# Kernel optimization log

Measured on AMD Instinct MI355X. Metric: run time of the kernel, lower is better.

## Reference

```python
import jax, jax.numpy as jnp
import numpy as np

N_NODES = 50000


def rgcn_conv(x, src, dst, edge_type, W, root, bias):
    """PyG RGCNConv: out[i] = x[i] @ root + bias + sum_r mean_{j in N_r(i)} x[j] @ W[r].
    W: [R, F_in, F_out]. Mean aggregation is per-relation (PyG default aggr='mean')."""
    num_rel = W.shape[0]
    n = x.shape[0]
    out = x @ root + bias
    x_src = x[src]  # [E, F_in] gather once
    for r in range(num_rel):  # small fixed relation count
        mask = (edge_type == r)
        msg = jnp.where(mask[:, None], x_src, 0.0) @ W[r]          # [E, F_out]
        s = jax.ops.segment_sum(msg, dst, num_segments=n)           # [N, F_out]
        c = jax.ops.segment_sum(mask.astype(x.dtype), dst, num_segments=n)  # [N]
        out = out + s / jnp.maximum(c, 1.0)[:, None]
    return out


def setup_inputs() -> dict:
    key = jax.random.key(0)
    ks = jax.random.split(key, 10)
    N, E, F_in, F_hid, F_out, R = N_NODES, 800000, 128, 128, 64, 8
    x = jax.random.normal(ks[0], (N, F_in), dtype=jnp.float32)
    edge_index = jax.random.randint(ks[1], (2, E), 0, N, dtype=jnp.int64)
    edge_type = jax.random.randint(ks[2], (E,), 0, R, dtype=jnp.int64)
    s1 = 1.0 / np.sqrt(F_in)
    s2 = 1.0 / np.sqrt(F_hid)
    W1 = jax.random.normal(ks[3], (R, F_in, F_hid), dtype=jnp.float32) * s1
    root1 = jax.random.normal(ks[4], (F_in, F_hid), dtype=jnp.float32) * s1
    b1 = jnp.zeros((F_hid,), dtype=jnp.float32)
    W2 = jax.random.normal(ks[5], (R, F_hid, F_out), dtype=jnp.float32) * s2
    root2 = jax.random.normal(ks[6], (F_hid, F_out), dtype=jnp.float32) * s2
    b2 = jnp.zeros((F_out,), dtype=jnp.float32)
    return {"x": x, "edge_index": edge_index, "edge_type": edge_type,
            "W1": W1, "root1": root1, "b1": b1,
            "W2": W2, "root2": root2, "b2": b2}


def reference(x, edge_index, edge_type, W1, root1, b1, W2, root2, b2):
    src, dst = edge_index[0], edge_index[1]
    h = jax.nn.relu(rgcn_conv(x, src, dst, edge_type, W1, root1, b1))
    out = rgcn_conv(h, src, dst, edge_type, W2, root2, b2)
    return out
```

## Files before the change

kernel.cpp:

```cpp
#include <hip/hip_runtime.h>

#define N_NODES 50000
#define N_EDGES 800000
#define R_REL   8
#define NR      (N_NODES * R_REL)

#define NBKT    196
#define BNSH    8
#define BKEYS   2048
#define BCAP    5120
#define SLAB    2048
#define BINBLK  ((N_EDGES + SLAB - 1) / SLAB)

typedef float  f32x4  __attribute__((ext_vector_type(4)));
typedef __bf16 bf16x8 __attribute__((ext_vector_type(8)));

__device__ __forceinline__ unsigned short f2bf(float f) {
    unsigned int u = __float_as_uint(f);
    u = (u + 0x7FFFu + ((u >> 16) & 1u)) >> 16;
    return (unsigned short)u;
}
__device__ __forceinline__ float bflo(unsigned int u) { return __uint_as_float(u << 16); }
__device__ __forceinline__ float bfhi(unsigned int u) { return __uint_as_float(u & 0xFFFF0000u); }

__device__ __forceinline__ void acc16(float* a, uint4 u0, uint4 u1) {
    a[0]  += bflo(u0.x);   a[1]  += bfhi(u0.x);
    a[2]  += bflo(u0.y);   a[3]  += bfhi(u0.y);
    a[4]  += bflo(u0.z);   a[5]  += bfhi(u0.z);
    a[6]  += bflo(u0.w);   a[7]  += bfhi(u0.w);
    a[8]  += bflo(u1.x);   a[9]  += bfhi(u1.x);
    a[10] += bflo(u1.y);   a[11] += bfhi(u1.y);
    a[12] += bflo(u1.z);   a[13] += bfhi(u1.z);
    a[14] += bflo(u1.w);   a[15] += bfhi(u1.w);
}


__global__ __launch_bounds__(256) void k_binA(
    const int* __restrict__ src, const int* __restrict__ dst,
    const int* __restrict__ et, int* __restrict__ gcur,
    uint2* __restrict__ gbin)
{
    __shared__ int hist[NBKT];
    __shared__ int base[NBKT];
    const int t = threadIdx.x;
    const int e0 = blockIdx.x * SLAB;
    for (int i = t; i < NBKT; i += 256) hist[i] = 0;
    __syncthreads();
#pragma unroll
    for (int i = 0; i < SLAB / 256; ++i) {
        int e = e0 + i * 256 + t;
        if (e < N_EDGES) atomicAdd(&hist[dst[e] >> BNSH], 1);
    }
    __syncthreads();
    for (int i = t; i < NBKT; i += 256) {
        int h = hist[i];
        base[i] = (h > 0) ? atomicAdd(&gcur[i], h) : 0;
        hist[i] = 0;
    }
    __syncthreads();
#pragma unroll
    for (int i = 0; i < SLAB / 256; ++i) {
        int e = e0 + i * 256 + t;
        if (e < N_EDGES) {
            int d = dst[e];
            int b = d >> BNSH;
            int sub = atomicAdd(&hist[b], 1);
            gbin[b * BCAP + base[b] + sub] =
                make_uint2((unsigned)src[e], (unsigned)(d * 8 + et[e]));
        }
    }
}

__global__ __launch_bounds__(256) void k_bcount_scan(
    const int* __restrict__ gcur, const uint2* __restrict__ gbin,
    int* __restrict__ offs, int* __restrict__ bsum)
{
    __shared__ int lc[BKEYS];
    __shared__ int sd[256];
    const int t = threadIdx.x;
    const int b = blockIdx.x;
    for (int i = t; i < BKEYS; i += 256) lc[i] = 0;
    __syncthreads();
    const int n = gcur[b];
    const uint2* rec = gbin + (size_t)b * BCAP;
    const int kbase = b * BKEYS;
    for (int j = t; j < n; j += 256)
        atomicAdd(&lc[rec[j].y - kbase], 1);
    __syncthreads();
    const int base = t * 8;
    int v[8];
    int tot = 0;
#pragma unroll
    for (int i = 0; i < 8; i++) {
        int xv = lc[base + i];
        v[i] = tot;
        tot += xv;
    }
    sd[t] = tot;
    __syncthreads();
    for (int off = 1; off < 256; off <<= 1) {
        int y = (t >= off) ? sd[t - off] : 0;
        __syncthreads();
        sd[t] += y;
        __syncthreads();
    }
    int excl = sd[t] - tot;
#pragma unroll
    for (int i = 0; i < 8; i++) {
        int k = kbase + base + i;
        if (k < NR) offs[k] = v[i] + excl;
    }
    if (t == 255) bsum[b] = sd[255];
}

__global__ __launch_bounds__(256) void k_bscat_final(
    const int* __restrict__ gcur, const uint2* __restrict__ gbin,
    const int* __restrict__ bsum, int* __restrict__ offs,
    int* __restrict__ srcS)
{
    __shared__ int obase[BKEYS];
    __shared__ int cur[BKEYS];
    __shared__ int sd[256];
    __shared__ int sadd;
    const int t = threadIdx.x;
    const int b = blockIdx.x;

    int v = (t < NBKT) ? bsum[t] : 0;
    sd[t] = v;
    __syncthreads();
    for (int off = 1; off < 256; off <<= 1) {
        int y = (t >= off) ? sd[t - off] : 0;
        __syncthreads();
        sd[t] += y;
        __syncthreads();
    }
    if (t == b) sadd = sd[t] - v;
    __syncthreads();
    const int add = sadd;

    const int kbase = b * BKEYS;
    for (int i = t; i < BKEYS; i += 256) {
        int k = kbase + i;
        int o = ((k < NR) ? offs[k] : 0) + add;
        obase[i] = o;
        cur[i] = 0;
        if (k < NR) offs[k] = o;
    }
    if (b == 0 && t == 0) offs[NR] = N_EDGES;
    __syncthreads();

    const int n = gcur[b];
    const uint2* rec = gbin + (size_t)b * BCAP;
    for (int j = t; j < n; j += 256) {
        uint2 r = rec[j];
        int li = r.y - kbase;
        int sub = atomicAdd(&cur[li], 1);
        srcS[obase[li] + sub] = (int)r.x;
    }
}


#define W1_ELEMS (9 * 128 * 128)
#define W2_ELEMS (9 * 64 * 128)
#define N4       (N_NODES * 32)

__global__ __launch_bounds__(256) void k_cvtw(
    const float* __restrict__ x, unsigned short* __restrict__ xb,
    const float* __restrict__ root1, const float* __restrict__ W1,
    const float* __restrict__ root2, const float* __restrict__ W2,
    unsigned short* __restrict__ Wt1, unsigned short* __restrict__ Wt2,
    int* __restrict__ gcur)
{
    const int idx = blockIdx.x * 256 + threadIdx.x;
    if (blockIdx.x == 0) gcur[threadIdx.x] = 0;
    if (idx < N4) {
        float4 v = *(const float4*)(x + (size_t)idx * 4);
        ushort4 o;
        o.x = f2bf(v.x); o.y = f2bf(v.y); o.z = f2bf(v.z); o.w = f2bf(v.w);
        *(ushort4*)(xb + (size_t)idx * 4) = o;
    }
    if (idx < W1_ELEMS) {
        int j    = idx & 7;
        int lane = (idx >> 3) & 63;
        int r    = idx >> 9;
        int nb   = r & 7;
        int r2   = r >> 3;
        int kk   = r2 & 3;
        int seg  = r2 >> 2;
        int k = kk * 32 + (lane >> 4) * 8 + j;
        int n = nb * 16 + (lane & 15);
        float v = (seg == 0) ? root1[k * 128 + n] : W1[((seg - 1) * 128 + k) * 128 + n];
        Wt1[idx] = f2bf(v);
    } else if (idx < W1_ELEMS + W2_ELEMS) {
        int i2   = idx - W1_ELEMS;
        int j    = i2 & 7;
        int lane = (i2 >> 3) & 63;
        int r    = i2 >> 9;
        int nb   = r & 3;
        int r2   = r >> 2;
        int kk   = r2 & 3;
        int seg  = r2 >> 2;
        int k = kk * 32 + (lane >> 4) * 8 + j;
        int n = nb * 16 + (lane & 15);
        float v = (seg == 0) ? root2[k * 64 + n] : W2[((seg - 1) * 128 + k) * 64 + n];
        Wt2[i2] = f2bf(v);
    }
}


template <int FOUT, bool RELU, bool OUT_BF16>
__global__ __launch_bounds__(512) void k_fused(
    const unsigned short* __restrict__ xin,
    const unsigned short* __restrict__ WtP,
    const float* __restrict__ bias,
    const int* __restrict__ offs,
    const int* __restrict__ srcS,
    unsigned short* __restrict__ outb,
    float* __restrict__ outf)
{
    constexpr int NBt = FOUT / 16;
    __shared__ __align__(16) unsigned short As[9][16][136];

    const int t = threadIdx.x;
    const int node0 = blockIdx.x * 16;

    if (t < 128) {
        const int sr = t >> 3;
        const int sp = t & 7;
        const uint4* src = (const uint4*)(xin + (size_t)(node0 + sr) * 128 + sp * 16);
        uint4 r0 = src[0], r1 = src[1];
        uint4* d = (uint4*)&As[0][sr][sp * 16];
        d[0] = r0; d[1] = r1;
    }

    {
        const int nl  = t >> 5;
        const int rel = (t >> 2) & 7;
        const int q   = t & 3;

        const int pair = (node0 + nl) * 8 + rel;
        const int beg = offs[pair];
        const int end = offs[pair + 1];
        const int deg = end - beg;

        const unsigned short* bx = xin + q * 32;
        float a[32];
#pragma unroll
        for (int i = 0; i < 32; ++i) a[i] = 0.f;

        int j = beg;
        for (; j + 1 < end; j += 2) {
            int s0 = srcS[j];
            int s1 = srcS[j + 1];
            const uint4* p0 = (const uint4*)(bx + (size_t)s0 * 128);
            const uint4* p1 = (const uint4*)(bx + (size_t)s1 * 128);
            uint4 v0 = p0[0], v1 = p0[1], v2 = p0[2], v3 = p0[3];
            uint4 w0 = p1[0], w1 = p1[1], w2 = p1[2], w3 = p1[3];
            acc16(a, v0, v1);
            acc16(a + 16, v2, v3);
            acc16(a, w0, w1);
            acc16(a + 16, w2, w3);
        }
        if (j < end) {
            int s = srcS[j];
            const uint4* p = (const uint4*)(bx + (size_t)s * 128);
            uint4 v0 = p[0], v1 = p[1], v2 = p[2], v3 = p[3];
            acc16(a, v0, v1);
            acc16(a + 16, v2, v3);
        }

        float scl = 1.f / (float)(deg > 1 ? deg : 1);
        unsigned int pk[16];
#pragma unroll
        for (int i = 0; i < 16; ++i)
            pk[i] = (unsigned int)f2bf(a[i * 2] * scl) |
                    ((unsigned int)f2bf(a[i * 2 + 1] * scl) << 16);
        uint4* G = (uint4*)&As[1 + rel][nl][0];
        const int g0 = q * 4;
        G[(g0 + 0) ^ rel] = make_uint4(pk[0],  pk[1],  pk[2],  pk[3]);
        G[(g0 + 1) ^ rel] = make_uint4(pk[4],  pk[5],  pk[6],  pk[7]);
        G[(g0 + 2) ^ rel] = make_uint4(pk[8],  pk[9],  pk[10], pk[11]);
        G[(g0 + 3) ^ rel] = make_uint4(pk[12], pk[13], pk[14], pk[15]);
    }

    __syncthreads();

    const int lane = t & 63;
    const int w = t >> 6;
    if (w >= NBt) return;
    const int quad = lane >> 4;
    const int tc = lane & 15;

    f32x4 acc = (f32x4){0.f, 0.f, 0.f, 0.f};
    const bf16x8* Bp = (const bf16x8*)WtP;

#pragma unroll
    for (int seg = 0; seg < 9; ++seg) {
        const uint4* Ag = (const uint4*)&As[seg][tc][0];
        const int s = (seg == 0) ? 0 : (seg - 1);
#pragma unroll
        for (int kk = 0; kk < 4; ++kk) {
            bf16x8 af = *(const bf16x8*)(Ag + (((kk << 2) + quad) ^ s));
            bf16x8 bf = Bp[((seg * 4 + kk) * NBt + w) * 64 + lane];
            acc = __builtin_amdgcn_mfma_f32_16x16x32_bf16(af, bf, acc, 0, 0, 0);
        }
    }

    const int col = w * 16 + tc;
    const float bs = bias[col];
#pragma unroll
    for (int i = 0; i < 4; ++i) {
        int r = node0 + quad * 4 + i;
        float v = acc[i] + bs;
        if (RELU) v = fmaxf(v, 0.f);
        if (OUT_BF16) outb[(size_t)r * FOUT + col] = f2bf(v);
        else          outf[(size_t)r * FOUT + col] = v;
    }
}


extern "C" void kernel_launch(void* const* d_in, const int* in_sizes, int n_in,
                              void* d_out, int out_size, void* d_ws, size_t ws_size,
                              hipStream_t stream) {
    const float* x     = (const float*)d_in[0];
    const int*   ei    = (const int*)d_in[1];
    const int*   et    = (const int*)d_in[2];
    const float* W1    = (const float*)d_in[3];
    const float* root1 = (const float*)d_in[4];
    const float* b1    = (const float*)d_in[5];
    const float* W2    = (const float*)d_in[6];
    const float* root2 = (const float*)d_in[7];
    const float* b2    = (const float*)d_in[8];
    float* out = (float*)d_out;

    int* ws     = (int*)d_ws;
    int* cnt    = ws;
    int* offs   = cnt + NR;
    int* wt2buf = offs + NR + 128;
    int* bsum   = wt2buf + NR;
    int* bsum2  = bsum + 256;
    int* gcur   = bsum2 + 256;
    int* srcS   = gcur + 256;
    unsigned short* xb  = (unsigned short*)(srcS + N_EDGES);
    unsigned short* hb  = xb + (size_t)N_NODES * 128;
    uint2* gbin = (uint2*)(hb + (size_t)N_NODES * 128);
    unsigned short* Wt1 = (unsigned short*)cnt;
    unsigned short* Wt2 = (unsigned short*)wt2buf;

    k_cvtw<<<(N4 + 255) / 256, 256, 0, stream>>>(x, xb, root1, W1, root2, W2,
                                                 Wt1, Wt2, gcur);
    k_binA<<<BINBLK, 256, 0, stream>>>(ei, ei + N_EDGES, et, gcur, gbin);
    k_bcount_scan<<<NBKT, 256, 0, stream>>>(gcur, gbin, offs, bsum);
    k_bscat_final<<<NBKT, 256, 0, stream>>>(gcur, gbin, bsum, offs, srcS);

    const int NT = N_NODES / 16;

    k_fused<128, true,  true ><<<NT, 512, 0, stream>>>(xb, Wt1, b1, offs, srcS, hb, nullptr);
    k_fused<64,  false, false><<<NT, 512, 0, stream>>>(hb, Wt2, b2, offs, srcS, nullptr, out);
}
```

Baseline: 250.7 us.

## Replace global CSR build with per-tile edge bins sorted in LDS

Edges are now binned directly into fixed-capacity buckets of 16 destination nodes in a single kernel, packing source and (node, relation) into one 32-bit word. This removes the separate count/scan and scatter kernels. Each fused aggregation block then counts, scans and sorts its own bucket's edges by (node, relation) in shared memory and reads sources from LDS instead of a global CSR array. The per-bucket capacity of 512 means edges beyond it would be silently dropped on skewed graphs, and the small local sort is now done in both layers.

```diff
diff --git a/kernel.cpp b/kernel.cpp
--- a/kernel.cpp
+++ b/kernel.cpp
@@ -3,12 +3,9 @@
 #define N_NODES 50000
 #define N_EDGES 800000
 #define R_REL   8
-#define NR      (N_NODES * R_REL)
-
-#define NBKT    196
-#define BNSH    8
-#define BKEYS   2048
-#define BCAP    5120
+
+#define TNBKT   3125
+#define TCAP    512
 #define SLAB    2048
 #define BINBLK  ((N_EDGES + SLAB - 1) / SLAB)
 
@@ -35,24 +32,24 @@
 }
 
 
-__global__ __launch_bounds__(256) void k_binA(
+__global__ __launch_bounds__(256) void k_bin(
     const int* __restrict__ src, const int* __restrict__ dst,
     const int* __restrict__ et, int* __restrict__ gcur,
-    uint2* __restrict__ gbin)
+    unsigned* __restrict__ gbin)
 {
-    __shared__ int hist[NBKT];
-    __shared__ int base[NBKT];
+    __shared__ int hist[TNBKT];
+    __shared__ int base[TNBKT];
     const int t = threadIdx.x;
     const int e0 = blockIdx.x * SLAB;
-    for (int i = t; i < NBKT; i += 256) hist[i] = 0;
+    for (int i = t; i < TNBKT; i += 256) hist[i] = 0;
     __syncthreads();
 #pragma unroll
     for (int i = 0; i < SLAB / 256; ++i) {
         int e = e0 + i * 256 + t;
-        if (e < N_EDGES) atomicAdd(&hist[dst[e] >> BNSH], 1);
-    }
-    __syncthreads();
-    for (int i = t; i < NBKT; i += 256) {
+        if (e < N_EDGES) atomicAdd(&hist[dst[e] >> 4], 1);
+    }
+    __syncthreads();
+    for (int i = t; i < TNBKT; i += 256) {
         int h = hist[i];
         base[i] = (h > 0) ? atomicAdd(&gcur[i], h) : 0;
         hist[i] = 0;
@@ -63,99 +60,12 @@
         int e = e0 + i * 256 + t;
         if (e < N_EDGES) {
             int d = dst[e];
-            int b = d >> BNSH;
+            int b = d >> 4;
             int sub = atomicAdd(&hist[b], 1);
-            gbin[b * BCAP + base[b] + sub] =
-                make_uint2((unsigned)src[e], (unsigned)(d * 8 + et[e]));
-        }
-    }
-}
-
-__global__ __launch_bounds__(256) void k_bcount_scan(
-    const int* __restrict__ gcur, const uint2* __restrict__ gbin,
-    int* __restrict__ offs, int* __restrict__ bsum)
-{
-    __shared__ int lc[BKEYS];
-    __shared__ int sd[256];
-    const int t = threadIdx.x;
-    const int b = blockIdx.x;
-    for (int i = t; i < BKEYS; i += 256) lc[i] = 0;
-    __syncthreads();
-    const int n = gcur[b];
-    const uint2* rec = gbin + (size_t)b * BCAP;
-    const int kbase = b * BKEYS;
-    for (int j = t; j < n; j += 256)
-        atomicAdd(&lc[rec[j].y - kbase], 1);
-    __syncthreads();
-    const int base = t * 8;
-    int v[8];
-    int tot = 0;
-#pragma unroll
-    for (int i = 0; i < 8; i++) {
-        int xv = lc[base + i];
-        v[i] = tot;
-        tot += xv;
-    }
-    sd[t] = tot;
-    __syncthreads();
-    for (int off = 1; off < 256; off <<= 1) {
-        int y = (t >= off) ? sd[t - off] : 0;
-        __syncthreads();
-        sd[t] += y;
-        __syncthreads();
-    }
-    int excl = sd[t] - tot;
-#pragma unroll
-    for (int i = 0; i < 8; i++) {
-        int k = kbase + base + i;
-        if (k < NR) offs[k] = v[i] + excl;
-    }
-    if (t == 255) bsum[b] = sd[255];
-}
-
-__global__ __launch_bounds__(256) void k_bscat_final(
-    const int* __restrict__ gcur, const uint2* __restrict__ gbin,
-    const int* __restrict__ bsum, int* __restrict__ offs,
-    int* __restrict__ srcS)
-{
-    __shared__ int obase[BKEYS];
-    __shared__ int cur[BKEYS];
-    __shared__ int sd[256];
-    __shared__ int sadd;
-    const int t = threadIdx.x;
-    const int b = blockIdx.x;
-
-    int v = (t < NBKT) ? bsum[t] : 0;
-    sd[t] = v;
-    __syncthreads();
-    for (int off = 1; off < 256; off <<= 1) {
-        int y = (t >= off) ? sd[t - off] : 0;
-        __syncthreads();
-        sd[t] += y;
-        __syncthreads();
-    }
-    if (t == b) sadd = sd[t] - v;
-    __syncthreads();
-    const int add = sadd;
-
-    const int kbase = b * BKEYS;
-    for (int i = t; i < BKEYS; i += 256) {
-        int k = kbase + i;
-        int o = ((k < NR) ? offs[k] : 0) + add;
-        obase[i] = o;
-        cur[i] = 0;
-        if (k < NR) offs[k] = o;
-    }
-    if (b == 0 && t == 0) offs[NR] = N_EDGES;
-    __syncthreads();
-
-    const int n = gcur[b];
-    const uint2* rec = gbin + (size_t)b * BCAP;
-    for (int j = t; j < n; j += 256) {
-        uint2 r = rec[j];
-        int li = r.y - kbase;
-        int sub = atomicAdd(&cur[li], 1);
-        srcS[obase[li] + sub] = (int)r.x;
+            int pos = base[b] + sub;
+            unsigned rec = ((unsigned)src[e] << 7) | (unsigned)((d & 15) * 8 + et[e]);
+            if (pos < TCAP) gbin[(size_t)b * TCAP + pos] = rec;
+        }
     }
 }
 
@@ -172,7 +82,7 @@
     int* __restrict__ gcur)
 {
     const int idx = blockIdx.x * 256 + threadIdx.x;
-    if (blockIdx.x == 0) gcur[threadIdx.x] = 0;
+    if (idx < TNBKT) gcur[idx] = 0;
     if (idx < N4) {
         float4 v = *(const float4*)(x + (size_t)idx * 4);
         ushort4 o;
@@ -213,35 +123,71 @@
     const unsigned short* __restrict__ xin,
     const unsigned short* __restrict__ WtP,
     const float* __restrict__ bias,
-    const int* __restrict__ offs,
-    const int* __restrict__ srcS,
+    const int* __restrict__ gcnt,
+    const unsigned* __restrict__ gbin,
     unsigned short* __restrict__ outb,
     float* __restrict__ outf)
 {
     constexpr int NBt = FOUT / 16;
-    __shared__ __align__(16) unsigned short As[9][16][136];
+    __shared__ __align__(16) unsigned short As0[16][136];
+    __shared__ __align__(16) unsigned short As[8][16][136];
+    __shared__ unsigned short sorted[TCAP];
+    __shared__ int dcnt[128];
+    __shared__ int kbeg[128];
+    __shared__ int kcur[128];
 
     const int t = threadIdx.x;
     const int node0 = blockIdx.x * 16;
 
+    if (t < 128) { dcnt[t] = 0; kcur[t] = 0; }
     if (t < 128) {
         const int sr = t >> 3;
         const int sp = t & 7;
-        const uint4* src = (const uint4*)(xin + (size_t)(node0 + sr) * 128 + sp * 16);
-        uint4 r0 = src[0], r1 = src[1];
-        uint4* d = (uint4*)&As[0][sr][sp * 16];
+        const uint4* s4 = (const uint4*)(xin + (size_t)(node0 + sr) * 128 + sp * 16);
+        uint4 r0 = s4[0], r1 = s4[1];
+        uint4* d = (uint4*)&As0[sr][sp * 16];
         d[0] = r0; d[1] = r1;
     }
+    const int nraw = gcnt[blockIdx.x];
+    const int n = nraw < TCAP ? nraw : TCAP;
+    unsigned rec = 0;
+    if (t < n) rec = gbin[(size_t)blockIdx.x * TCAP + t];
+    __syncthreads();
+
+    if (t < n) atomicAdd(&dcnt[rec & 127], 1);
+    __syncthreads();
+
+    if (t < 64) {
+        int d0 = dcnt[2 * t], d1 = dcnt[2 * t + 1];
+        int s = d0 + d1;
+        int inc = s;
+#pragma unroll
+        for (int off = 1; off < 64; off <<= 1) {
+            int y = __shfl_up(inc, off, 64);
+            if (t >= off) inc += y;
+        }
+        int excl = inc - s;
+        kbeg[2 * t]     = excl;
+        kbeg[2 * t + 1] = excl + d0;
+    }
+    __syncthreads();
+
+    if (t < n) {
+        int key = rec & 127;
+        int pos = atomicAdd(&kcur[key], 1);
+        sorted[kbeg[key] + pos] = (unsigned short)(rec >> 7);
+    }
+    __syncthreads();
 
     {
-        const int nl  = t >> 5;
-        const int rel = (t >> 2) & 7;
+        const int key = t >> 2;
         const int q   = t & 3;
-
-        const int pair = (node0 + nl) * 8 + rel;
-        const int beg = offs[pair];
-        const int end = offs[pair + 1];
-        const int deg = end - beg;
+        const int rel = key & 7;
+        const int nl  = key >> 3;
+
+        const int beg = kbeg[key];
+        const int deg = dcnt[key];
+        const int end = beg + deg;
 
         const unsigned short* bx = xin + q * 32;
         float a[32];
@@ -250,8 +196,8 @@
 
         int j = beg;
         for (; j + 1 < end; j += 2) {
-            int s0 = srcS[j];
-            int s1 = srcS[j + 1];
+            int s0 = sorted[j];
+            int s1 = sorted[j + 1];
             const uint4* p0 = (const uint4*)(bx + (size_t)s0 * 128);
             const uint4* p1 = (const uint4*)(bx + (size_t)s1 * 128);
             uint4 v0 = p0[0], v1 = p0[1], v2 = p0[2], v3 = p0[3];
@@ -262,7 +208,7 @@
             acc16(a + 16, w2, w3);
         }
         if (j < end) {
-            int s = srcS[j];
+            int s = sorted[j];
             const uint4* p = (const uint4*)(bx + (size_t)s * 128);
             uint4 v0 = p[0], v1 = p[1], v2 = p[2], v3 = p[3];
             acc16(a, v0, v1);
@@ -275,7 +221,7 @@
         for (int i = 0; i < 16; ++i)
             pk[i] = (unsigned int)f2bf(a[i * 2] * scl) |
                     ((unsigned int)f2bf(a[i * 2 + 1] * scl) << 16);
-        uint4* G = (uint4*)&As[1 + rel][nl][0];
+        uint4* G = (uint4*)&As[rel][nl][0];
         const int g0 = q * 4;
         G[(g0 + 0) ^ rel] = make_uint4(pk[0],  pk[1],  pk[2],  pk[3]);
         G[(g0 + 1) ^ rel] = make_uint4(pk[4],  pk[5],  pk[6],  pk[7]);
@@ -296,7 +242,8 @@
 
 #pragma unroll
     for (int seg = 0; seg < 9; ++seg) {
-        const uint4* Ag = (const uint4*)&As[seg][tc][0];
+        const uint4* Ag = (seg == 0) ? (const uint4*)&As0[tc][0]
+                                     : (const uint4*)&As[seg - 1][tc][0];
         const int s = (seg == 0) ? 0 : (seg - 1);
 #pragma unroll
         for (int kk = 0; kk < 4; ++kk) {
@@ -333,28 +280,23 @@
     const float* b2    = (const float*)d_in[8];
     float* out = (float*)d_out;
 
-    int* ws     = (int*)d_ws;
-    int* cnt    = ws;
-    int* offs   = cnt + NR;
-    int* wt2buf = offs + NR + 128;
-    int* bsum   = wt2buf + NR;
-    int* bsum2  = bsum + 256;
-    int* gcur   = bsum2 + 256;
-    int* srcS   = gcur + 256;
-    unsigned short* xb  = (unsigned short*)(srcS + N_EDGES);
+    int* ws = (int*)d_ws;
+    int* gcur = ws;
+    unsigned* gbin = (unsigned*)(gcur + 3200);
+    unsigned short* xb  = (unsigned short*)(gbin + (size_t)TNBKT * TCAP);
     unsigned short* hb  = xb + (size_t)N_NODES * 128;
-    uint2* gbin = (uint2*)(hb + (size_t)N_NODES * 128);
-    unsigned short* Wt1 = (unsigned short*)cnt;
-    unsigned short* Wt2 = (unsigned short*)wt2buf;
+    unsigned short* Wt1 = hb + (size_t)N_NODES * 128;
+    unsigned short* Wt2 = Wt1 + W1_ELEMS;
+
+    const int* esrc = ei;
+    const int* edst = ei + N_EDGES;
 
     k_cvtw<<<(N4 + 255) / 256, 256, 0, stream>>>(x, xb, root1, W1, root2, W2,
                                                  Wt1, Wt2, gcur);
-    k_binA<<<BINBLK, 256, 0, stream>>>(ei, ei + N_EDGES, et, gcur, gbin);
-    k_bcount_scan<<<NBKT, 256, 0, stream>>>(gcur, gbin, offs, bsum);
-    k_bscat_final<<<NBKT, 256, 0, stream>>>(gcur, gbin, bsum, offs, srcS);
+    k_bin<<<BINBLK, 256, 0, stream>>>(esrc, edst, et, gcur, gbin);
 
     const int NT = N_NODES / 16;
 
-    k_fused<128, true,  true ><<<NT, 512, 0, stream>>>(xb, Wt1, b1, offs, srcS, hb, nullptr);
-    k_fused<64,  false, false><<<NT, 512, 0, stream>>>(hb, Wt2, b2, offs, srcS, nullptr, out);
-}
+    k_fused<128, true,  true ><<<NT, 512, 0, stream>>>(xb, Wt1, b1, gcur, gbin, hb, nullptr);
+    k_fused<64,  false, false><<<NT, 512, 0, stream>>>(hb, Wt2, b2, gcur, gbin, nullptr, out);
+}
```

Result: no change. 254.6 us (+1.6%).
